# Performance work log

Hardware: AMD Instinct MI355X
Metric: run time of the kernel (lower is better)

## Reference

```python
import jax, jax.numpy as jnp
import numpy as np

R = 32  # voxel resolution
B, CIN, COUT, N = 4, 64, 64, 4096
K = 3


def setup_inputs():
    key = jax.random.key(0)
    ks = jax.random.split(key, 8)
    s = 0.05
    return {
        "features": jax.random.normal(ks[0], (B, CIN, N), jnp.float32),
        "coords": jax.random.normal(ks[1], (B, 3, N), jnp.float32),
        # voxel branch: conv3d + BN x2
        "w1": jax.random.normal(ks[2], (COUT, CIN, K, K, K), jnp.float32) * s,
        "b1": jnp.zeros((COUT,), jnp.float32),
        "g1": jnp.ones((COUT,), jnp.float32),
        "be1": jnp.zeros((COUT,), jnp.float32),
        "w2": jax.random.normal(ks[3], (COUT, COUT, K, K, K), jnp.float32) * s,
        "b2": jnp.zeros((COUT,), jnp.float32),
        "g2": jnp.ones((COUT,), jnp.float32),
        "be2": jnp.zeros((COUT,), jnp.float32),
        # point branch SharedMLP (1x1 conv + BN + ReLU)
        "wp": jax.random.normal(ks[4], (COUT, CIN), jnp.float32) * s,
        "bp": jnp.zeros((COUT,), jnp.float32),
        "gp": jnp.ones((COUT,), jnp.float32),
        "bep": jnp.zeros((COUT,), jnp.float32),
        # fuzzy_proj 1x1 conv
        "wf": jax.random.normal(ks[5], (COUT, CIN), jnp.float32) * s,
        "bf": jnp.zeros((COUT,), jnp.float32),
        # fusion SharedMLP (3*COUT -> COUT)
        "wfu": jax.random.normal(ks[6], (COUT, 3 * COUT), jnp.float32) * s,
        "bfu": jnp.zeros((COUT,), jnp.float32),
        "gfu": jnp.ones((COUT,), jnp.float32),
        "befu": jnp.zeros((COUT,), jnp.float32),
    }


def _bn3d(x, g, b):
    # training-mode BatchNorm3d, eps=1e-4 (biased variance, as torch)
    m = x.mean((0, 2, 3, 4), keepdims=True)
    v = x.var((0, 2, 3, 4), keepdims=True)
    return (x - m) * jax.lax.rsqrt(v + 1e-4) * g[None, :, None, None, None] + b[None, :, None, None, None]


def _bn1d(x, g, b):
    m = x.mean((0, 2), keepdims=True)
    v = x.var((0, 2), keepdims=True)
    return (x - m) * jax.lax.rsqrt(v + 1e-4) * g[None, :, None] + b[None, :, None]


def _conv3d(x, w, b):
    pad = K // 2
    y = jax.lax.conv_general_dilated(x, w, (1, 1, 1), [(pad, pad)] * 3,
                                     dimension_numbers=('NCDHW', 'OIDHW', 'NCDHW'))
    return y + b[None, :, None, None, None]


def _conv1x1(x, w, b):
    return jnp.einsum('oc,bcn->bon', w, x) + b[None, :, None]


def _voxelize(features, coords):
    # PVCNN Voxelization(normalize=True, eps=0): center, scale to unit, grid coords in [0, R-1]
    nc = coords - coords.mean(axis=2, keepdims=True)              # [B,3,N]
    norm = jnp.linalg.norm(nc, axis=1, keepdims=True)             # [B,1,N]
    nc = nc / (norm.max(axis=2, keepdims=True) * 2.0) + 0.5
    nc = jnp.clip(nc * R, 0.0, R - 1)
    vox = jnp.round(nc).astype(jnp.int32)                         # [B,3,N]
    b_, c_, n_ = features.shape
    idx = (vox[:, 0] * R + vox[:, 1]) * R + vox[:, 2]             # [B,N]
    flat = (idx + jnp.arange(b_)[:, None] * R ** 3).reshape(-1)
    feat = features.transpose(0, 2, 1).reshape(b_ * n_, c_)
    sums = jax.ops.segment_sum(feat, flat, num_segments=b_ * R ** 3)
    cnt = jax.ops.segment_sum(jnp.ones((b_ * n_,), feat.dtype), flat, num_segments=b_ * R ** 3)
    avg = sums / jnp.maximum(cnt, 1.0)[:, None]                   # scatter-mean
    grid = avg.reshape(b_, R ** 3, c_).transpose(0, 2, 1).reshape(b_, c_, R, R, R)
    return grid, nc


def _devoxelize(grid, nc):
    # trilinear gather: grid [B,C,R,R,R], nc [B,3,N] float coords in [0,R-1]
    b_, c_ = grid.shape[:2]
    g = grid.reshape(b_, c_, -1)
    lo_f = jnp.floor(nc)
    fr = nc - lo_f                                                # fractional part [B,3,N]
    lo = lo_f.astype(jnp.int32)
    hi = jnp.minimum(lo + 1, R - 1)
    out = jnp.zeros((b_, c_, nc.shape[2]), grid.dtype)
    for dx in (0, 1):
        for dy in (0, 1):
            for dz in (0, 1):
                ix = hi[:, 0] if dx else lo[:, 0]
                iy = hi[:, 1] if dy else lo[:, 1]
                iz = hi[:, 2] if dz else lo[:, 2]
                w = ((fr[:, 0] if dx else 1.0 - fr[:, 0]) *
                     (fr[:, 1] if dy else 1.0 - fr[:, 1]) *
                     (fr[:, 2] if dz else 1.0 - fr[:, 2]))        # [B,N]
                flat = (ix * R + iy) * R + iz                     # [B,N]
                vals = jnp.take_along_axis(g, flat[:, None, :], axis=2)  # [B,C,N]
                out = out + vals * w[:, None, :]
    return out


def reference(features, coords, w1, b1, g1, be1, w2, b2, g2, be2,
              wp, bp, gp, bep, wf, bf, wfu, bfu, gfu, befu):
    lrelu = lambda x: jnp.where(x > 0, x, 0.1 * x)
    # voxel branch
    grid, nc = _voxelize(features, coords)
    v = lrelu(_bn3d(_conv3d(grid, w1, b1), g1, be1))
    v = lrelu(_bn3d(_conv3d(v, w2, b2), g2, be2))
    vox_feat = _devoxelize(v, nc)                                 # [B,COUT,N]
    # point branch
    pt = jax.nn.relu(_bn1d(_conv1x1(features, wp, bp), gp, bep))
    # fuzzy branch: dense attention over points
    cn = coords.transpose(0, 2, 1)                                # [B,N,3]
    cn = cn / jnp.maximum(jnp.linalg.norm(cn, axis=-1, keepdims=True), 1e-12)
    att = jax.nn.softmax(jnp.einsum('bnd,bmd->bnm', cn, cn) / 0.1, axis=-1)
    fz = jnp.einsum('bnm,bcm->bcn', att, features)                # [B,CIN,N]
    fz = _conv1x1(fz, wf, bf)
    # fusion
    comb = jnp.concatenate([vox_feat, pt, fz], axis=1)            # [B,3*COUT,N]
    fused = jax.nn.relu(_bn1d(_conv1x1(comb, wfu, bfu), gfu, befu))
    return (fused, coords)
```

## Files before the change

### kernel.cpp

```cpp
#include <hip/hip_runtime.h>
#include <hip/hip_bf16.h>
#include <math.h>

#define RR 32
#define R3 32768
#define BB 4
#define CI 64
#define CO 64
#define NN 4096

typedef short v8s __attribute__((ext_vector_type(8)));
typedef float v4f __attribute__((ext_vector_type(4)));
typedef unsigned short ushort_t;

__device__ __forceinline__ unsigned short f2bf(float f) {
    unsigned int u = __float_as_uint(f);
    unsigned int r = (u + 0x7FFFu + ((u >> 16) & 1u)) >> 16;
    return (unsigned short)r;
}
__device__ __forceinline__ float bf2f(unsigned short h) {
    return __uint_as_float((unsigned int)h << 16);
}

__device__ __forceinline__ void gll16(const void* g, void* l) {
    __builtin_amdgcn_global_load_lds((const __attribute__((address_space(1))) unsigned int*)g,
                                     (__attribute__((address_space(3))) unsigned int*)l, 16, 0, 0);
}

__device__ __forceinline__ float blockReduceSum(float v, float* sm) {
    int tid = threadIdx.x;
    sm[tid] = v; __syncthreads();
    for (int off = 128; off > 0; off >>= 1) {
        if (tid < off) sm[tid] += sm[tid + off];
        __syncthreads();
    }
    float r = sm[0]; __syncthreads();
    return r;
}
__device__ __forceinline__ float blockReduceMax(float v, float* sm) {
    int tid = threadIdx.x;
    sm[tid] = v; __syncthreads();
    for (int off = 128; off > 0; off >>= 1) {
        if (tid < off) sm[tid] = fmaxf(sm[tid], sm[tid + off]);
        __syncthreads();
    }
    float r = sm[0]; __syncthreads();
    return r;
}

__global__ void k_nc(const float* __restrict__ coords, float* __restrict__ nc,
                     int* __restrict__ vidx, int* __restrict__ cntI) {
    int b = blockIdx.x, tid = threadIdx.x;
    __shared__ float sm[256];
    const float* cb = coords + (size_t)b * 3 * NN;
    float s0 = 0, s1 = 0, s2 = 0;
    for (int n = tid; n < NN; n += 256) {
        s0 += cb[n]; s1 += cb[NN + n]; s2 += cb[2 * NN + n];
    }
    float m0 = blockReduceSum(s0, sm) * (1.0f / NN);
    float m1 = blockReduceSum(s1, sm) * (1.0f / NN);
    float m2 = blockReduceSum(s2, sm) * (1.0f / NN);
    float mx = 0;
    for (int n = tid; n < NN; n += 256) {
        float dx = cb[n] - m0, dy = cb[NN + n] - m1, dz = cb[2 * NN + n] - m2;
        mx = fmaxf(mx, dx * dx + dy * dy + dz * dz);
    }
    mx = blockReduceMax(mx, sm);
    float denom = 2.0f * sqrtf(mx);
    float mean[3] = {m0, m1, m2};
    for (int n = tid; n < NN; n += 256) {
        int vi[3];
        #pragma unroll
        for (int ax = 0; ax < 3; ax++) {
            float x = (cb[ax * NN + n] - mean[ax]) / denom + 0.5f;
            x = x * RR;
            x = fminf(fmaxf(x, 0.0f), (float)(RR - 1));
            nc[((size_t)b * 3 + ax) * NN + n] = x;
            vi[ax] = (int)rintf(x);
        }
        int idx = (vi[0] * RR + vi[1]) * RR + vi[2];
        vidx[b * NN + n] = idx;
        atomicAdd(&cntI[b * R3 + idx], 1);
    }
}

__global__ void k_scan1(const int* __restrict__ cntI, int* __restrict__ lscan,
                        int* __restrict__ bsum) {
    __shared__ int sm[256];
    int tid = threadIdx.x;
    int i = blockIdx.x * 256 + tid;
    int v = cntI[i];
    sm[tid] = v; __syncthreads();
    for (int off = 1; off < 256; off <<= 1) {
        int t = (tid >= off) ? sm[tid - off] : 0;
        __syncthreads();
        sm[tid] += t;
        __syncthreads();
    }
    lscan[i] = sm[tid] - v;
    if (tid == 255) bsum[blockIdx.x] = sm[tid];
}

__global__ void k_scan2(const int* __restrict__ bsum, int* __restrict__ bbase) {
    __shared__ int sm[512];
    int tid = threadIdx.x;
    int v = bsum[tid];
    sm[tid] = v; __syncthreads();
    for (int off = 1; off < 512; off <<= 1) {
        int t = (tid >= off) ? sm[tid - off] : 0;
        __syncthreads();
        sm[tid] += t;
        __syncthreads();
    }
    bbase[tid] = sm[tid] - v;
}

__global__ void k_fill(const int* __restrict__ vidx, const int* __restrict__ lscan,
                       const int* __restrict__ bbase, int* __restrict__ rank,
                       int* __restrict__ plist) {
    int i = blockIdx.x * 256 + threadIdx.x;
    int b = i >> 12, n = i & (NN - 1);
    int flat = b * R3 + vidx[i];
    int r = atomicAdd(&rank[flat], 1);
    plist[bbase[flat >> 8] + lscan[flat] + r] = n;
}

__global__ void k_tfcl(const float* __restrict__ feat, float* __restrict__ featT) {
    __shared__ float t[64][65];
    int b = blockIdx.y, n0 = blockIdx.x * 64, tid = threadIdx.x;
    int q = tid >> 6, nl = tid & 63;
    #pragma unroll
    for (int k = 0; k < 16; k++) {
        int c = q * 16 + k;
        t[nl][c] = feat[((size_t)(b * CI + c)) * NN + n0 + nl];
    }
    __syncthreads();
    #pragma unroll
    for (int k = 0; k < 16; k++) {
        int n = q * 16 + k;
        featT[((size_t)b * NN + n0 + n) * 64 + nl] = t[n][nl];
    }
}

__global__ __launch_bounds__(256) void k_gather(const float* __restrict__ featT,
                                                const int* __restrict__ cntI,
                                                const int* __restrict__ lscan,
                                                const int* __restrict__ bbase,
                                                const int* __restrict__ plist,
                                                ushort_t* __restrict__ gT) {
    int wv = threadIdx.x >> 6, lane = threadIdx.x & 63;
    int vbase = blockIdx.x * 32 + wv * 8;
    for (int k = 0; k < 8; k++) {
        int flat = vbase + k;
        int count = cntI[flat];
        float s = 0.0f;
        if (count > 0) {
            int b = flat >> 15;
            int start = bbase[flat >> 8] + lscan[flat];
            for (int j = 0; j < count; j++) {
                int n = plist[start + j];
                s += featT[((size_t)b * NN + n) * 64 + lane];
            }
            s *= 1.0f / (float)count;
        }
        gT[(size_t)flat * 64 + lane] = f2bf(s);
    }
}

__global__ void k_f2b(const float* __restrict__ x, ushort_t* __restrict__ o) {
    size_t i = (size_t)blockIdx.x * 256 + threadIdx.x;
    float4 a = ((const float4*)x)[i * 2];
    float4 b = ((const float4*)x)[i * 2 + 1];
    union { __hip_bfloat162 h[4]; uint4 u; } pk;
    pk.h[0] = __float22bfloat162_rn(make_float2(a.x, a.y));
    pk.h[1] = __float22bfloat162_rn(make_float2(a.z, a.w));
    pk.h[2] = __float22bfloat162_rn(make_float2(b.x, b.y));
    pk.h[3] = __float22bfloat162_rn(make_float2(b.z, b.w));
    ((uint4*)o)[i] = pk.u;
}

__global__ void k_tws(const float* __restrict__ w, ushort_t* __restrict__ wS) {
    int i = blockIdx.x * 256 + threadIdx.x;
    int cis = i & 31, co = (i >> 5) & 63;
    int dx = (i >> 11) % 3, cih = (i / 6144) & 1, dzdy = i / 12288;
    int k = dzdy * 3 + dx, ci = cih * 32 + cis;
    wS[i] = f2bf(w[((size_t)co * CI + ci) * 27 + k]);
}

__global__ void k_fold(const float* __restrict__ wp, const float* __restrict__ wfu,
                       const float* __restrict__ wf, const float* __restrict__ bf,
                       const float* __restrict__ bfu,
                       float* __restrict__ wpT, float* __restrict__ wfuT,
                       float* __restrict__ bC) {
    int i = blockIdx.x * 256 + threadIdx.x;
    if (i < 4096) {
        int c = i >> 6, o = i & 63;
        wpT[c * 64 + o] = wp[o * 64 + c];
    } else if (i < 12288) {
        int j = i - 4096;
        int c = j >> 6, o = j & 63;
        wfuT[c * 64 + o] = wfu[(size_t)o * 192 + c];
    } else if (i < 16384) {
        int j = i - 12288;
        int c = j >> 6, o = j & 63;
        float s = 0;
        for (int k = 0; k < 64; k++)
            s += wfu[(size_t)o * 192 + 128 + k] * wf[(size_t)k * 64 + c];
        wfuT[(128 + c) * 64 + o] = s;
    } else if (i < 16448) {
        int o = i - 16384;
        float s = bfu[o];
        for (int k = 0; k < 64; k++)
            s += wfu[(size_t)o * 192 + 128 + k] * bf[k];
        bC[o] = s;
    }
}

__global__ void k_bncast2(const ushort_t* __restrict__ x, const float* __restrict__ accs,
                          const float* __restrict__ g, const float* __restrict__ be,
                          float invcnt, float slope, ushort_t* __restrict__ o) {
    size_t i = (size_t)blockIdx.x * 256 + threadIdx.x;
    int c0 = (int)((i * 8) & 63);
    float sc[8], sh[8];
    #pragma unroll
    for (int j = 0; j < 8; j++) {
        int c = c0 + j;
        float mean = accs[2 * c] * invcnt;
        float var = accs[2 * c + 1] * invcnt - mean * mean;
        float scale = g[c] * rsqrtf(var + 1e-4f);
        sc[j] = scale;
        sh[j] = be[c] - mean * scale;
    }
    uint4 in = ((const uint4*)x)[i];
    unsigned iv[4] = {in.x, in.y, in.z, in.w};
    unsigned pk[4];
    #pragma unroll
    for (int j = 0; j < 4; j++) {
        float u0 = bf2f((unsigned short)(iv[j] & 0xFFFF)) * sc[2 * j] + sh[2 * j];
        float u1 = bf2f((unsigned short)(iv[j] >> 16)) * sc[2 * j + 1] + sh[2 * j + 1];
        u0 = u0 > 0 ? u0 : slope * u0;
        u1 = u1 > 0 ? u1 : slope * u1;
        pk[j] = (unsigned)f2bf(u0) | ((unsigned)f2bf(u1) << 16);
    }
    ((uint4*)o)[i] = make_uint4(pk[0], pk[1], pk[2], pk[3]);
}

template <int OUTBF16>
__global__ __launch_bounds__(256) void k_convlds(const ushort_t* __restrict__ gT,
                                                 const ushort_t* __restrict__ wS,
                                                 void* __restrict__ outP,
                                                 float* __restrict__ accs) {
    __shared__ ushort_t lin[20480];
    __shared__ ushort_t lw[6144];
    int bid = blockIdx.x;
    int wgid = (bid & 7) * 64 + (bid >> 3);
    int yt = wgid & 3, z0 = (wgid >> 2) & 31, b = wgid >> 7;
    int tid = threadIdx.x;
    int w = __builtin_amdgcn_readfirstlane(tid >> 6);
    int lane = tid & 63, l15 = lane & 15, l4 = lane >> 4;
    int y0 = yt * 8;
    const ushort_t* gTb = gT + (size_t)b * R3 * 64;

    int voxF[4];
    #pragma unroll
    for (int f = 0; f < 4; f++)
        voxF[f] = (w * 2 + (f >> 1)) * 32 + (f & 1) * 16 + l15 - 1;
    bool xlo_ok = (l15 != 0), xhi_ok = (l15 != 15);

    const v8s vzero = {};
    v4f acc[4][4];
    #pragma unroll
    for (int m = 0; m < 4; m++)
        #pragma unroll
        for (int f = 0; f < 4; f++)
            acc[m][f] = (v4f){0.0f, 0.0f, 0.0f, 0.0f};

#define WSTAGE(s)                                                              \
    do {                                                                       \
        const ushort_t* _src = wS + (size_t)(s) * 6144;                        \
        _Pragma("unroll") for (int _i = 0; _i < 3; _i++) {                     \
            int _p = _i * 256 + w * 64;                                        \
            gll16(_src + (size_t)(_p + lane) * 8, lw + (size_t)_p * 8);        \
        }                                                                      \
    } while (0)

#define ISTAGE(dz)                                                             \
    do {                                                                       \
        int _zp = z0 - 1 + (dz);                                               \
        if (_zp < 0 || _zp > 31) {                                             \
            for (int _q = 0; _q < 10; _q++)                                    \
                *(v8s*)&lin[(size_t)(w * 640 + _q * 64 + lane) * 8] = vzero;   \
        } else {                                                               \
            if (yt == 0) *(v8s*)&lin[(size_t)tid * 8] = vzero;                 \
            if (yt == 3) *(v8s*)&lin[(size_t)(2304 + tid) * 8] = vzero;        \
            const ushort_t* _pb = gTb + ((size_t)_zp * 1024 + (size_t)(y0 - 1) * 32) * 64; \
            int _g0 = (yt == 0) ? 256 : 0;                                     \
            int _nc = 10 - (yt == 0) - (yt == 3);                              \
            for (int _i = 0; _i < _nc; _i++) {                                 \
                int _pbase = _g0 + _i * 256 + w * 64;                          \
                int _p = _pbase + lane;                                        \
                int _vx = _p >> 3, _js = _p & 7;                               \
                int _sg = _vx * 8 + (_js ^ (_vx & 7));                         \
                gll16(_pb + (size_t)_sg * 8, lin + (size_t)_pbase * 8);        \
            }                                                                  \
        }                                                                      \
    } while (0)

    for (int s = 0; s < 18; s++) {
        int dy = (s / 2) % 3, cih = s & 1;
        asm volatile("s_barrier" ::: "memory");
        if ((s % 6) == 0) ISTAGE(s / 6);
        WSTAGE(s);
        asm volatile("s_waitcnt vmcnt(0) lgkmcnt(0)" ::: "memory");
        asm volatile("s_barrier" ::: "memory");

        #pragma unroll
        for (int dx = 0; dx < 3; dx++) {
            v8s Bf[4];
            #pragma unroll
            for (int f = 0; f < 4; f++) {
                int vox = voxF[f] + dy * 32 + dx;
                int g = vox * 8 + ((cih * 4 + l4) ^ (vox & 7));
                int bix = g * 16;
                bix = bix < 0 ? 0 : bix;
                v8s vb = *(const v8s*)((const char*)lin + bix);
                bool ok = (dx == 0 && (f & 1) == 0) ? xlo_ok :
                          (dx == 2 && (f & 1) == 1) ? xhi_ok : true;
                Bf[f] = ok ? vb : vzero;
            }
            const ushort_t* ap = lw + dx * 2048 + l15 * 32 + l4 * 8;
            #pragma unroll
            for (int m = 0; m < 4; m++) {
                v8s Af = *(const v8s*)(ap + m * 512);
                #pragma unroll
                for (int f = 0; f < 4; f++)
                    acc[m][f] = __builtin_amdgcn_mfma_f32_16x16x32_bf16(Af, Bf[f], acc[m][f], 0, 0, 0);
            }
        }
    }

    #pragma unroll
    for (int m = 0; m < 4; m++) {
        #pragma unroll
        for (int f = 0; f < 4; f++) {
            int y = y0 + w * 2 + (f >> 1);
            int x = (f & 1) * 16 + l15;
            size_t base = ((size_t)b * R3 + z0 * 1024 + y * 32 + x) * 64 + m * 16 + l4 * 4;
            if (OUTBF16) {
                unsigned p0 = (unsigned)f2bf(acc[m][f][0]) | ((unsigned)f2bf(acc[m][f][1]) << 16);
                unsigned p1 = (unsigned)f2bf(acc[m][f][2]) | ((unsigned)f2bf(acc[m][f][3]) << 16);
                *(uint2*)&((ushort_t*)outP)[base] = make_uint2(p0, p1);
            } else {
                float4 o = make_float4(acc[m][f][0], acc[m][f][1], acc[m][f][2], acc[m][f][3]);
                *(float4*)&((float*)outP)[base] = o;
            }
        }
    }

    __syncthreads();
    float* sbuf = (float*)lin;
    #pragma unroll
    for (int m = 0; m < 4; m++)
        #pragma unroll
        for (int r = 0; r < 4; r++) {
            float s = 0, q = 0;
            #pragma unroll
            for (int f = 0; f < 4; f++) {
                float v = acc[m][f][r];
                s += v; q += v * v;
            }
            sbuf[tid * 32 + (m * 4 + r) * 2] = s;
            sbuf[tid * 32 + (m * 4 + r) * 2 + 1] = q;
        }
    __syncthreads();
    if (tid < 128) {
        int co = tid >> 1, val = tid & 1;
        int m = co >> 4, cl4 = (co >> 2) & 3, r = co & 3;
        float a = 0;
        for (int w2 = 0; w2 < 4; w2++)
            for (int l = 0; l < 16; l++)
                a += sbuf[(w2 * 64 + cl4 * 16 + l) * 32 + (m * 4 + r) * 2 + val];
        atomicAdd(&accs[2 * co + val], a);
    }
#undef WSTAGE
#undef ISTAGE
}

__global__ void k_bnfin2(const float* __restrict__ pst, const float* __restrict__ g,
                         const float* __restrict__ be, float* __restrict__ stats,
                         float invcnt) {
    int c = blockIdx.x, tid = threadIdx.x;
    __shared__ float rs[256], rq[256];
    rs[tid] = pst[(c * 256 + tid) * 2];
    rq[tid] = pst[(c * 256 + tid) * 2 + 1];
    __syncthreads();
    for (int off = 128; off > 0; off >>= 1) {
        if (tid < off) { rs[tid] += rs[tid + off]; rq[tid] += rq[tid + off]; }
        __syncthreads();
    }
    if (tid == 0) {
        float mean = rs[0] * invcnt;
        float var = rq[0] * invcnt - mean * mean;
        float sc = g[c] * rsqrtf(var + 1e-4f);
        stats[2 * c] = sc;
        stats[2 * c + 1] = be[c] - mean * sc;
    }
}

__global__ void k_bn_act(const float* __restrict__ x, const float* __restrict__ stats,
                         float* __restrict__ out, int shift, float slope) {
    size_t i = (size_t)blockIdx.x * 256 + threadIdx.x;
    int c = (int)((i >> shift) & 63);
    float sc = stats[2 * c], sh = stats[2 * c + 1];
    float4 v = ((const float4*)x)[i];
    v.x = v.x * sc + sh; v.y = v.y * sc + sh; v.z = v.z * sc + sh; v.w = v.w * sc + sh;
    v.x = v.x > 0 ? v.x : slope * v.x;
    v.y = v.y > 0 ? v.y : slope * v.y;
    v.z = v.z > 0 ? v.z : slope * v.z;
    v.w = v.w > 0 ? v.w : slope * v.w;
    ((float4*)out)[i] = v;
}

__global__ void k_devox2(const float* __restrict__ gcl, const float* __restrict__ accs,
                         const float* __restrict__ g, const float* __restrict__ be,
                         float invcnt, const float* __restrict__ nc,
                         float* __restrict__ out) {
    int b = blockIdx.y;
    int tid = threadIdx.x, p = tid >> 4, q = tid & 15;
    int n = blockIdx.x * 16 + p;
    float x = nc[((size_t)b * 3 + 0) * NN + n];
    float y = nc[((size_t)b * 3 + 1) * NN + n];
    float z = nc[((size_t)b * 3 + 2) * NN + n];
    float fx = floorf(x), fy = floorf(y), fz = floorf(z);
    int lx = (int)fx, ly = (int)fy, lz = (int)fz;
    int hx = min(lx + 1, RR - 1), hy = min(ly + 1, RR - 1), hz = min(lz + 1, RR - 1);
    float frx = x - fx, fry = y - fy, frz = z - fz;
    int xx[2] = {lx, hx}, yy[2] = {ly, hy}, zz[2] = {lz, hz};
    float wx[2] = {1.0f - frx, frx}, wy[2] = {1.0f - fry, fry}, wz[2] = {1.0f - frz, frz};
    float sc[4], sh[4];
    #pragma unroll
    for (int j = 0; j < 4; j++) {
        int c = q * 4 + j;
        float mean = accs[2 * c] * invcnt;
        float var = accs[2 * c + 1] * invcnt - mean * mean;
        float scale = g[c] * rsqrtf(var + 1e-4f);
        sc[j] = scale;
        sh[j] = be[c] - mean * scale;
    }
    float a0 = 0, a1 = 0, a2 = 0, a3 = 0;
    #pragma unroll
    for (int dx = 0; dx < 2; dx++)
        #pragma unroll
        for (int dy = 0; dy < 2; dy++)
            #pragma unroll
            for (int dz = 0; dz < 2; dz++) {
                int idx = (xx[dx] * RR + yy[dy]) * RR + zz[dz];
                float wt = wx[dx] * wy[dy] * wz[dz];
                float4 v = *(const float4*)&gcl[((size_t)b * R3 + idx) * 64 + q * 4];
                float u0 = v.x * sc[0] + sh[0]; u0 = u0 > 0 ? u0 : 0.1f * u0;
                float u1 = v.y * sc[1] + sh[1]; u1 = u1 > 0 ? u1 : 0.1f * u1;
                float u2 = v.z * sc[2] + sh[2]; u2 = u2 > 0 ? u2 : 0.1f * u2;
                float u3 = v.w * sc[3] + sh[3]; u3 = u3 > 0 ? u3 : 0.1f * u3;
                a0 += wt * u0; a1 += wt * u1; a2 += wt * u2; a3 += wt * u3;
            }
    out[((size_t)(b * 64 + q * 4 + 0)) * NN + n] = a0;
    out[((size_t)(b * 64 + q * 4 + 1)) * NN + n] = a1;
    out[((size_t)(b * 64 + q * 4 + 2)) * NN + n] = a2;
    out[((size_t)(b * 64 + q * 4 + 3)) * NN + n] = a3;
}

__global__ __launch_bounds__(256) void k_fuzzym(const float* __restrict__ coords,
                                                const ushort_t* __restrict__ featb,
                                                float* __restrict__ pnum,
                                                float* __restrict__ pden) {
    __shared__ float cm[3][1024];
    __shared__ ushort_t la[2][2048];
    int b = blockIdx.z, mc = blockIdx.y, nt = blockIdx.x;
    int tid = threadIdx.x;
    int w = tid >> 6, lane = tid & 63, l15 = lane & 15, l4 = lane >> 4;
    int m0 = mc * 1024;

    for (int i = tid; i < 1024; i += 256) {
        float a0 = coords[((size_t)b * 3 + 0) * NN + m0 + i];
        float a1 = coords[((size_t)b * 3 + 1) * NN + m0 + i];
        float a2 = coords[((size_t)b * 3 + 2) * NN + m0 + i];
        float inv = 1.0f / fmaxf(sqrtf(a0 * a0 + a1 * a1 + a2 * a2), 1e-12f);
        cm[0][i] = a0 * inv; cm[1][i] = a1 * inv; cm[2][i] = a2 * inv;
    }

    int n = nt * 64 + w * 16 + l15;
    float q0 = coords[((size_t)b * 3 + 0) * NN + n];
    float q1 = coords[((size_t)b * 3 + 1) * NN + n];
    float q2 = coords[((size_t)b * 3 + 2) * NN + n];
    float qi = 10.0f / fmaxf(sqrtf(q0 * q0 + q1 * q1 + q2 * q2), 1e-12f);
    q0 *= qi; q1 *= qi; q2 *= qi;

    int srow = tid >> 2, sslot = tid & 3;
    int g0 = sslot ^ ((srow >> 1) & 3);
    const ushort_t* fb = featb + (size_t)b * 64 * NN + m0;
    const ushort_t* sbase = fb + (size_t)srow * NN + g0 * 8;
    int rsw = (l15 >> 1) & 3;

    v4f acc[4];
    #pragma unroll
    for (int cb = 0; cb < 4; cb++) acc[cb] = (v4f){0.0f, 0.0f, 0.0f, 0.0f};
    float den = 0.0f;

    gll16(sbase, &la[0][(size_t)tid * 8]);
    asm volatile("s_waitcnt vmcnt(0)" ::: "memory");
    __syncthreads();

    for (int t = 0; t < 32; t++) {
        int cur = t & 1;
        if (t + 1 < 32)
            gll16(sbase + (t + 1) * 32, &la[cur ^ 1][(size_t)tid * 8]);

        int mo = t * 32 + l4 * 8;
        float e[8];
        #pragma unroll
        for (int jj = 0; jj < 2; jj++) {
            float4 x0 = *(const float4*)&cm[0][mo + jj * 4];
            float4 x1 = *(const float4*)&cm[1][mo + jj * 4];
            float4 x2 = *(const float4*)&cm[2][mo + jj * 4];
            e[jj * 4 + 0] = __expf(q0 * x0.x + q1 * x1.x + q2 * x2.x);
            e[jj * 4 + 1] = __expf(q0 * x0.y + q1 * x1.y + q2 * x2.y);
            e[jj * 4 + 2] = __expf(q0 * x0.z + q1 * x1.z + q2 * x2.z);
            e[jj * 4 + 3] = __expf(q0 * x0.w + q1 * x1.w + q2 * x2.w);
        }
        den += ((e[0] + e[1]) + (e[2] + e[3])) + ((e[4] + e[5]) + (e[6] + e[7]));
        union { __hip_bfloat162 h[4]; v8s v; } pk;
        pk.h[0] = __float22bfloat162_rn(make_float2(e[0], e[1]));
        pk.h[1] = __float22bfloat162_rn(make_float2(e[2], e[3]));
        pk.h[2] = __float22bfloat162_rn(make_float2(e[4], e[5]));
        pk.h[3] = __float22bfloat162_rn(make_float2(e[6], e[7]));
        #pragma unroll
        for (int cb = 0; cb < 4; cb++) {
            v8s A = *(const v8s*)&la[cur][(size_t)((cb * 16 + l15) * 4 + (l4 ^ rsw)) * 8];
            acc[cb] = __builtin_amdgcn_mfma_f32_16x16x32_bf16(A, pk.v, acc[cb], 0, 0, 0);
        }
        asm volatile("s_waitcnt vmcnt(0)" ::: "memory");
        __syncthreads();
    }

    den += __shfl_xor(den, 16);
    den += __shfl_xor(den, 32);

    size_t obase = ((size_t)(b * 4 + mc)) * 64 * NN;
    #pragma unroll
    for (int cb = 0; cb < 4; cb++)
        #pragma unroll
        for (int r = 0; r < 4; r++)
            pnum[obase + (size_t)(cb * 16 + l4 * 4 + r) * NN + n] = acc[cb][r];
    if (l4 == 0) pden[((size_t)(b * 4 + mc)) * NN + n] = den;
}

__global__ void k_combine2(const float* __restrict__ pnum, const float* __restrict__ pden,
                           float* __restrict__ fzf) {
    int i = blockIdx.x * 256 + threadIdx.x;
    int b = i >> 18, c = (i >> 12) & 63, n = i & 4095;
    float num = 0, den = 0;
    #pragma unroll
    for (int ch = 0; ch < 4; ch++) {
        num += pnum[((size_t)(b * 4 + ch) * 64 + c) * NN + n];
        den += pden[((size_t)(b * 4 + ch)) * NN + n];
    }
    fzf[((size_t)(b * 64 + c)) * NN + n] = num / den;
}

__global__ __launch_bounds__(256) void k_1x1s(const float* __restrict__ in,
                                              const float* __restrict__ wT,
                                              const float* __restrict__ bias,
                                              float* __restrict__ out,
                                              float* __restrict__ pst) {
    int b = blockIdx.z, ob = blockIdx.y, bx = blockIdx.x;
    int tid = threadIdx.x;
    int q = tid & 15, o = ob * 16 + (tid >> 4);
    int n = bx * 64 + q * 4;
    const float* src = in + (size_t)b * 64 * NN + n;
    const float* wp_ = wT + o;
    v4f acc = {0, 0, 0, 0};
    #pragma unroll 8
    for (int c = 0; c < 64; c++) {
        float4 x = *(const float4*)&src[(size_t)c * NN];
        float w = wp_[c * 64];
        acc[0] += x.x * w; acc[1] += x.y * w; acc[2] += x.z * w; acc[3] += x.w * w;
    }
    float bv = bias[o];
    float s = 0, q2 = 0;
    float4 ov;
    float* op = (float*)&ov;
    #pragma unroll
    for (int v = 0; v < 4; v++) {
        float val = acc[v] + bv;
        op[v] = val;
        s += val; q2 += val * val;
    }
    *(float4*)&out[((size_t)(b * 64 + o)) * NN + n] = ov;
    #pragma unroll
    for (int off = 1; off < 16; off <<= 1) {
        s += __shfl_xor(s, off);
        q2 += __shfl_xor(q2, off);
    }
    if (q == 0) {
        int part = bx * 4 + b;
        pst[(o * 256 + part) * 2] = s;
        pst[(o * 256 + part) * 2 + 1] = q2;
    }
}

__global__ __launch_bounds__(256) void k_1x1f(const float* __restrict__ vox,
                                              const float* __restrict__ pt,
                                              const float* __restrict__ fzf,
                                              const float* __restrict__ bnB,
                                              const float* __restrict__ wfuT,
                                              const float* __restrict__ bC,
                                              float* __restrict__ out,
                                              float* __restrict__ pst) {
    int b = blockIdx.z, ob = blockIdx.y, bx = blockIdx.x;
    int tid = threadIdx.x;
    int q = tid & 15, o = ob * 16 + (tid >> 4);
    int n = bx * 64 + q * 4;
    const float* srcA = vox + (size_t)b * 64 * NN + n;
    const float* srcB = pt + (size_t)b * 64 * NN + n;
    const float* srcC = fzf + (size_t)b * 64 * NN + n;
    const float* wA = wfuT + o;
    v4f acc = {0, 0, 0, 0};
    #pragma unroll 8
    for (int c = 0; c < 64; c++) {
        float4 x = *(const float4*)&srcA[(size_t)c * NN];
        float w = wA[c * 64];
        acc[0] += x.x * w; acc[1] += x.y * w; acc[2] += x.z * w; acc[3] += x.w * w;
    }
    #pragma unroll 8
    for (int c = 0; c < 64; c++) {
        float4 x = *(const float4*)&srcB[(size_t)c * NN];
        float sc = bnB[2 * c], sh = bnB[2 * c + 1];
        float w = wA[(64 + c) * 64];
        float x0 = fmaxf(x.x * sc + sh, 0.0f), x1 = fmaxf(x.y * sc + sh, 0.0f);
        float x2 = fmaxf(x.z * sc + sh, 0.0f), x3 = fmaxf(x.w * sc + sh, 0.0f);
        acc[0] += x0 * w; acc[1] += x1 * w; acc[2] += x2 * w; acc[3] += x3 * w;
    }
    #pragma unroll 8
    for (int c = 0; c < 64; c++) {
        float4 x = *(const float4*)&srcC[(size_t)c * NN];
        float w = wA[(128 + c) * 64];
        acc[0] += x.x * w; acc[1] += x.y * w; acc[2] += x.z * w; acc[3] += x.w * w;
    }
    float bv = bC[o];
    float s = 0, q2 = 0;
    float4 ov;
    float* op = (float*)&ov;
    #pragma unroll
    for (int v = 0; v < 4; v++) {
        float val = acc[v] + bv;
        op[v] = val;
        s += val; q2 += val * val;
    }
    *(float4*)&out[((size_t)(b * 64 + o)) * NN + n] = ov;
    #pragma unroll
    for (int off = 1; off < 16; off <<= 1) {
        s += __shfl_xor(s, off);
        q2 += __shfl_xor(q2, off);
    }
    if (q == 0) {
        int part = bx * 4 + b;
        pst[(o * 256 + part) * 2] = s;
        pst[(o * 256 + part) * 2 + 1] = q2;
    }
}

extern "C" void kernel_launch(void* const* d_in, const int* in_sizes, int n_in,
                              void* d_out, int out_size, void* d_ws, size_t ws_size,
                              hipStream_t stream) {
    const float* features = (const float*)d_in[0];
    const float* coords = (const float*)d_in[1];
    const float* w1 = (const float*)d_in[2];
    const float* g1 = (const float*)d_in[4];
    const float* be1 = (const float*)d_in[5];
    const float* w2 = (const float*)d_in[6];
    const float* g2 = (const float*)d_in[8];
    const float* be2 = (const float*)d_in[9];
    const float* wp = (const float*)d_in[10];
    const float* bp = (const float*)d_in[11];
    const float* gp = (const float*)d_in[12];
    const float* bep = (const float*)d_in[13];
    const float* wf = (const float*)d_in[14];
    const float* bf = (const float*)d_in[15];
    const float* wfu = (const float*)d_in[16];
    const float* bfu = (const float*)d_in[17];
    const float* gfu = (const float*)d_in[18];
    const float* befu = (const float*)d_in[19];

    float* ws = (float*)d_ws;
    float* nc = ws;
    int* vidx = (int*)(ws + 49152);
    int* cntI = (int*)(ws + 65536);
    float* pden = ws + 65536;
    float* gridCL = ws + 196608;
    ushort_t* gTraw = (ushort_t*)gridCL;
    int* lscan = (int*)(ws + 196608);
    int* bsum = (int*)(ws + 327680);
    int* bbase = (int*)(ws + 328192);
    int* rank = (int*)(ws + 328704);
    int* plist = (int*)(ws + 459776);
    float* featT = ws + 476160;
    float* gTpool = ws + 8585216;
    ushort_t* gT = (ushort_t*)gTpool;
    float* pnum = gTpool;
    float* pstB = gTpool;
    float* stats = ws + 16973824;
    float* voxreg = ws + 16974336;
    ushort_t* wS1 = (ushort_t*)voxreg;
    ushort_t* wS2 = wS1 + 110592;
    float* vox = voxreg;
    float* pt = ws + 18022912;
    float* fzf = ws + 19071488;
    float* wpT = ws + 20120064;
    float* wfuT = wpT + 4096;
    float* bC = wfuT + 12288;
    float* fpre = ws + 21168640;
    ushort_t* featb = (ushort_t*)fpre;
    float* accs = ws + 22217216;

    float* out = (float*)d_out;

    hipMemsetAsync(accs, 0, 512 * 4, stream);
    hipMemsetAsync(cntI, 0, 131072 * 4, stream);
    hipMemsetAsync(rank, 0, 131072 * 4, stream);

    k_fold<<<65, 256, 0, stream>>>(wp, wfu, wf, bf, bfu, wpT, wfuT, bC);
    k_f2b<<<BB * 64 * NN / 8 / 256, 256, 0, stream>>>(features, featb);
    k_tws<<<432, 256, 0, stream>>>(w1, wS1);
    k_tws<<<432, 256, 0, stream>>>(w2, wS2);
    k_tfcl<<<dim3(64, BB), 256, 0, stream>>>(features, featT);

    k_nc<<<BB, 256, 0, stream>>>(coords, nc, vidx, cntI);
    k_scan1<<<512, 256, 0, stream>>>(cntI, lscan, bsum);
    k_scan2<<<1, 512, 0, stream>>>(bsum, bbase);
    k_fill<<<BB * NN / 256, 256, 0, stream>>>(vidx, lscan, bbase, rank, plist);
    k_gather<<<4096, 256, 0, stream>>>(featT, cntI, lscan, bbase, plist, gT);

    k_convlds<1><<<512, 256, 0, stream>>>(gT, wS1, gTraw, accs);
    k_bncast2<<<BB * R3 * 64 / 8 / 256, 256, 0, stream>>>(gTraw, accs, g1, be1,
                                                          1.0f / (BB * R3), 0.1f, gT);
    k_convlds<0><<<512, 256, 0, stream>>>(gT, wS2, gridCL, accs + 128);
    k_devox2<<<dim3(NN / 16, BB), 256, 0, stream>>>(gridCL, accs + 128, g2, be2,
                                                    1.0f / (BB * R3), nc, vox);

    k_fuzzym<<<dim3(64, 4, BB), 256, 0, stream>>>(coords, featb, pnum, pden);
    k_combine2<<<BB * 64 * NN / 256, 256, 0, stream>>>(pnum, pden, fzf);

    k_1x1s<<<dim3(NN / 64, 4, BB), 256, 0, stream>>>(features, wpT, bp, pt, pstB);
    k_bnfin2<<<64, 256, 0, stream>>>(pstB, gp, bep, stats + 256, 1.0f / (BB * NN));

    k_1x1f<<<dim3(NN / 64, 4, BB), 256, 0, stream>>>(vox, pt, fzf, stats + 256, wfuT, bC,
                                                     fpre, pstB);
    k_bnfin2<<<64, 256, 0, stream>>>(pstB, gfu, befu, stats + 384, 1.0f / (BB * NN));
    k_bn_act<<<BB * 64 * NN / 4 / 256, 256, 0, stream>>>(fpre, stats + 384, out, 10, 0.0f);

    hipMemcpyAsync(out + (size_t)BB * CO * NN, coords, (size_t)BB * 3 * NN * 4,
                   hipMemcpyDeviceToDevice, stream);
}
```

Baseline: 278.8 us.

## Register-prefetch conv weight stages and merge small preprocessing kernels and memsets

The conv kernel now prefetches the next weight stage into registers while computing the current one, writing it to a padded LDS layout (row stride 104) in place of synchronous global-to-LDS loads followed by a full vmcnt wait each stage. Separately, the bf16 feature cast is fused into the transpose kernel, the two weight-swizzle launches are merged into one, and the accs memset is folded into k_fold, with rank moved next to cntI so a single memset clears both. This aims to hide weight-load latency and cut launch overhead, at the cost of extra registers and a changed LDS layout.

```diff
diff --git a/kernel.cpp b/kernel.cpp
--- a/kernel.cpp
+++ b/kernel.cpp
@@ -125,14 +125,17 @@
     plist[bbase[flat >> 8] + lscan[flat] + r] = n;
 }
 
-__global__ void k_tfcl(const float* __restrict__ feat, float* __restrict__ featT) {
+__global__ void k_pfeat(const float* __restrict__ feat, float* __restrict__ featT,
+                        ushort_t* __restrict__ featb) {
     __shared__ float t[64][65];
     int b = blockIdx.y, n0 = blockIdx.x * 64, tid = threadIdx.x;
     int q = tid >> 6, nl = tid & 63;
     #pragma unroll
     for (int k = 0; k < 16; k++) {
         int c = q * 16 + k;
-        t[nl][c] = feat[((size_t)(b * CI + c)) * NN + n0 + nl];
+        float v = feat[((size_t)(b * CI + c)) * NN + n0 + nl];
+        t[nl][c] = v;
+        featb[((size_t)(b * CI + c)) * NN + n0 + nl] = f2bf(v);
     }
     __syncthreads();
     #pragma unroll
@@ -167,31 +170,23 @@
     }
 }
 
-__global__ void k_f2b(const float* __restrict__ x, ushort_t* __restrict__ o) {
-    size_t i = (size_t)blockIdx.x * 256 + threadIdx.x;
-    float4 a = ((const float4*)x)[i * 2];
-    float4 b = ((const float4*)x)[i * 2 + 1];
-    union { __hip_bfloat162 h[4]; uint4 u; } pk;
-    pk.h[0] = __float22bfloat162_rn(make_float2(a.x, a.y));
-    pk.h[1] = __float22bfloat162_rn(make_float2(a.z, a.w));
-    pk.h[2] = __float22bfloat162_rn(make_float2(b.x, b.y));
-    pk.h[3] = __float22bfloat162_rn(make_float2(b.z, b.w));
-    ((uint4*)o)[i] = pk.u;
-}
-
-__global__ void k_tws(const float* __restrict__ w, ushort_t* __restrict__ wS) {
+__global__ void k_tws(const float* __restrict__ w1, const float* __restrict__ w2,
+                      ushort_t* __restrict__ wS1, ushort_t* __restrict__ wS2) {
     int i = blockIdx.x * 256 + threadIdx.x;
-    int cis = i & 31, co = (i >> 5) & 63;
-    int dx = (i >> 11) % 3, cih = (i / 6144) & 1, dzdy = i / 12288;
+    const float* w = (i < 110592) ? w1 : w2;
+    ushort_t* wS = (i < 110592) ? wS1 : wS2;
+    int j = (i < 110592) ? i : i - 110592;
+    int cis = j & 31, co = (j >> 5) & 63;
+    int dx = (j >> 11) % 3, cih = (j / 6144) & 1, dzdy = j / 12288;
     int k = dzdy * 3 + dx, ci = cih * 32 + cis;
-    wS[i] = f2bf(w[((size_t)co * CI + ci) * 27 + k]);
+    wS[j] = f2bf(w[((size_t)co * CI + ci) * 27 + k]);
 }
 
 __global__ void k_fold(const float* __restrict__ wp, const float* __restrict__ wfu,
                        const float* __restrict__ wf, const float* __restrict__ bf,
                        const float* __restrict__ bfu,
                        float* __restrict__ wpT, float* __restrict__ wfuT,
-                       float* __restrict__ bC) {
+                       float* __restrict__ bC, float* __restrict__ accs) {
     int i = blockIdx.x * 256 + threadIdx.x;
     if (i < 4096) {
         int c = i >> 6, o = i & 63;
@@ -213,6 +208,8 @@
         for (int k = 0; k < 64; k++)
             s += wfu[(size_t)o * 192 + 128 + k] * bf[k];
         bC[o] = s;
+    } else if (i < 16960) {
+        accs[i - 16448] = 0.0f;
     }
 }
 
@@ -251,7 +248,7 @@
                                                  void* __restrict__ outP,
                                                  float* __restrict__ accs) {
     __shared__ ushort_t lin[20480];
-    __shared__ ushort_t lw[6144];
+    __shared__ ushort_t lw[6656];
     int bid = blockIdx.x;
     int wgid = (bid & 7) * 64 + (bid >> 3);
     int yt = wgid & 3, z0 = (wgid >> 2) & 31, b = wgid >> 7;
@@ -275,14 +272,11 @@
         for (int f = 0; f < 4; f++)
             acc[m][f] = (v4f){0.0f, 0.0f, 0.0f, 0.0f};
 
-#define WSTAGE(s)                                                              \
-    do {                                                                       \
-        const ushort_t* _src = wS + (size_t)(s) * 6144;                        \
-        _Pragma("unroll") for (int _i = 0; _i < 3; _i++) {                     \
-            int _p = _i * 256 + w * 64;                                        \
-            gll16(_src + (size_t)(_p + lane) * 8, lw + (size_t)_p * 8);        \
-        }                                                                      \
-    } while (0)
+    int co_s = tid >> 2, gr_s = tid & 3;
+    uint4 wreg[3];
+    #pragma unroll
+    for (int i = 0; i < 3; i++)
+        wreg[i] = *(const uint4*)(wS + (size_t)(i * 256 + tid) * 8);
 
 #define ISTAGE(dz)                                                             \
     do {                                                                       \
@@ -308,10 +302,22 @@
 
     for (int s = 0; s < 18; s++) {
         int dy = (s / 2) % 3, cih = s & 1;
+        (void)cih;
         asm volatile("s_barrier" ::: "memory");
         if ((s % 6) == 0) ISTAGE(s / 6);
-        WSTAGE(s);
-        asm volatile("s_waitcnt vmcnt(0) lgkmcnt(0)" ::: "memory");
+        #pragma unroll
+        for (int i = 0; i < 3; i++)
+            *(uint4*)&lw[co_s * 104 + (i * 4 + gr_s) * 8] = wreg[i];
+        if (s + 1 < 18) {
+            const ushort_t* src = wS + (size_t)(s + 1) * 6144;
+            #pragma unroll
+            for (int i = 0; i < 3; i++)
+                wreg[i] = *(const uint4*)(src + (size_t)(i * 256 + tid) * 8);
+        }
+        if ((s % 6) == 0)
+            asm volatile("s_waitcnt vmcnt(0) lgkmcnt(0)" ::: "memory");
+        else
+            asm volatile("s_waitcnt lgkmcnt(0)" ::: "memory");
         asm volatile("s_barrier" ::: "memory");
 
         #pragma unroll
@@ -320,7 +326,7 @@
             #pragma unroll
             for (int f = 0; f < 4; f++) {
                 int vox = voxF[f] + dy * 32 + dx;
-                int g = vox * 8 + ((cih * 4 + l4) ^ (vox & 7));
+                int g = vox * 8 + (((s & 1) * 4 + l4) ^ (vox & 7));
                 int bix = g * 16;
                 bix = bix < 0 ? 0 : bix;
                 v8s vb = *(const v8s*)((const char*)lin + bix);
@@ -328,10 +334,10 @@
                           (dx == 2 && (f & 1) == 1) ? xhi_ok : true;
                 Bf[f] = ok ? vb : vzero;
             }
-            const ushort_t* ap = lw + dx * 2048 + l15 * 32 + l4 * 8;
+            const ushort_t* ap = lw + l15 * 104 + (dx * 4 + l4) * 8;
             #pragma unroll
             for (int m = 0; m < 4; m++) {
-                v8s Af = *(const v8s*)(ap + m * 512);
+                v8s Af = *(const v8s*)(ap + m * 1664);
                 #pragma unroll
                 for (int f = 0; f < 4; f++)
                     acc[m][f] = __builtin_amdgcn_mfma_f32_16x16x32_bf16(Af, Bf[f], acc[m][f], 0, 0, 0);
@@ -382,7 +388,6 @@
                 a += sbuf[(w2 * 64 + cl4 * 16 + l) * 32 + (m * 4 + r) * 2 + val];
         atomicAdd(&accs[2 * co + val], a);
     }
-#undef WSTAGE
 #undef ISTAGE
 }
 
@@ -698,10 +703,10 @@
     float* pden = ws + 65536;
     float* gridCL = ws + 196608;
     ushort_t* gTraw = (ushort_t*)gridCL;
-    int* lscan = (int*)(ws + 196608);
-    int* bsum = (int*)(ws + 327680);
-    int* bbase = (int*)(ws + 328192);
-    int* rank = (int*)(ws + 328704);
+    int* rank = (int*)(ws + 196608);
+    int* lscan = (int*)(ws + 327680);
+    int* bsum = (int*)(ws + 458752);
+    int* bbase = (int*)(ws + 459264);
     int* plist = (int*)(ws + 459776);
     float* featT = ws + 476160;
     float* gTpool = ws + 8585216;
@@ -724,15 +729,11 @@
 
     float* out = (float*)d_out;
 
-    hipMemsetAsync(accs, 0, 512 * 4, stream);
-    hipMemsetAsync(cntI, 0, 131072 * 4, stream);
-    hipMemsetAsync(rank, 0, 131072 * 4, stream);
-
-    k_fold<<<65, 256, 0, stream>>>(wp, wfu, wf, bf, bfu, wpT, wfuT, bC);
-    k_f2b<<<BB * 64 * NN / 8 / 256, 256, 0, stream>>>(features, featb);
-    k_tws<<<432, 256, 0, stream>>>(w1, wS1);
-    k_tws<<<432, 256, 0, stream>>>(w2, wS2);
-    k_tfcl<<<dim3(64, BB), 256, 0, stream>>>(features, featT);
+    hipMemsetAsync(cntI, 0, (size_t)262144 * 4, stream);
+
+    k_fold<<<67, 256, 0, stream>>>(wp, wfu, wf, bf, bfu, wpT, wfuT, bC, accs);
+    k_pfeat<<<dim3(64, BB), 256, 0, stream>>>(features, featT, featb);
+    k_tws<<<864, 256, 0, stream>>>(w1, w2, wS1, wS2);
 
     k_nc<<<BB, 256, 0, stream>>>(coords, nc, vidx, cntI);
     k_scan1<<<512, 256, 0, stream>>>(cntI, lscan, bsum);
```

Measured after the change: 303.6 us. +8.9%, slower.
